# Kernel tuning notes

Hardware: AMD Instinct MI355X
Metric: run time of the kernel (lower is better)

## Reference

```python
import jax, jax.numpy as jnp
import numpy as np

D = 1280        # embed_dim
H = 20          # num heads
HD = D // H     # head_dim = 64
FFN = 5120
SEQ = 4096
NSEG = 8
EPS = 1e-5


def _ln(x, g, b):
    mu = jnp.mean(x, axis=-1, keepdims=True)
    var = jnp.var(x, axis=-1, keepdims=True)
    return (x - mu) * jax.lax.rsqrt(var + EPS) * g + b


def setup_inputs() -> dict:
    key = jax.random.key(0)
    ks = jax.random.split(key, 16)
    s = 0.02
    inp = {
        "hidden_states": jax.random.normal(ks[0], (SEQ, D), dtype=jnp.float32),
        "cu_seqlens": jnp.arange(NSEG + 1, dtype=jnp.int32) * (SEQ // NSEG),
        "Wq": jax.random.normal(ks[1], (D, D), dtype=jnp.float32) * s,
        "bq": jnp.zeros((D,), jnp.float32),
        "Wk": jax.random.normal(ks[2], (D, D), dtype=jnp.float32) * s,
        "Wv": jax.random.normal(ks[3], (D, D), dtype=jnp.float32) * s,
        "bv": jnp.zeros((D,), jnp.float32),
        "Wo": jax.random.normal(ks[4], (D, D), dtype=jnp.float32) * s,
        "bo": jnp.zeros((D,), jnp.float32),
        "ln1_g": jnp.ones((D,), jnp.float32),
        "ln1_b": jnp.zeros((D,), jnp.float32),
        "Wf1": jax.random.normal(ks[5], (D, FFN), dtype=jnp.float32) * s,
        "bf1": jnp.zeros((FFN,), jnp.float32),
        "Wf2": jax.random.normal(ks[6], (FFN, D), dtype=jnp.float32) * s,
        "bf2": jnp.zeros((D,), jnp.float32),
        "ln2_g": jnp.ones((D,), jnp.float32),
        "ln2_b": jnp.zeros((D,), jnp.float32),
    }
    return inp


def reference(hidden_states, cu_seqlens, Wq, bq, Wk, Wv, bv, Wo, bo,
              ln1_g, ln1_b, Wf1, bf1, Wf2, bf2, ln2_g, ln2_b):
    seq = hidden_states.shape[0]
    # --- self-attention block ---
    residual = hidden_states
    x = _ln(hidden_states, ln1_g, ln1_b)
    q = (x @ Wq + bq).reshape(seq, H, HD).transpose(1, 0, 2)   # [H,S,hd]
    k = (x @ Wk).reshape(seq, H, HD).transpose(1, 0, 2)
    v = (x @ Wv + bv).reshape(seq, H, HD).transpose(1, 0, 2)
    scores = jnp.einsum('hqd,hkd->hqk', q, k) / jnp.sqrt(jnp.float32(HD))
    # block-diagonal mask from cu_seqlens (segment id per token)
    pos = jnp.arange(seq, dtype=jnp.int32)
    seg = jnp.searchsorted(cu_seqlens, pos, side='right')      # [S]
    same = seg[None, :, None] == seg[None, None, :]            # [1,S,S]
    neg = jnp.finfo(scores.dtype).min
    scores = jnp.where(same, scores, scores + neg)
    attn = jax.nn.softmax(scores, axis=-1)
    attn_out = jnp.einsum('hqk,hkd->hqd', attn, v).transpose(1, 0, 2).reshape(seq, D)
    attn_out = attn_out @ Wo + bo
    h = residual + attn_out
    # --- FFN block ---
    residual = h
    y = _ln(h, ln2_g, ln2_b)
    y = jax.nn.gelu(y @ Wf1 + bf1, approximate=False)
    y = y @ Wf2 + bf2
    return residual + y
```

## Files before the change

kernel.cpp:

```cpp
#include <hip/hip_runtime.h>
#include <cstdint>
#include <cstddef>

#define SEQ_ 4096
#define DIM_ 1280
#define NHEAD_ 20
#define HDIM_ 64
#define FFN_ 5120
#define SEG_ 512
#define QKVN_ 3840

typedef __attribute__((ext_vector_type(8))) short bf16x8;
typedef __attribute__((ext_vector_type(4))) float f32x4;
typedef __attribute__((ext_vector_type(8))) unsigned short us8;
typedef __attribute__((ext_vector_type(4))) unsigned short us4;

__device__ __forceinline__ unsigned short f2b(float f) {
  unsigned int u = __builtin_bit_cast(unsigned int, f);
  u += 0x7fffu + ((u >> 16) & 1u);
  return (unsigned short)(u >> 16);
}

__device__ __forceinline__ float b2f(unsigned short u) {
  return __builtin_bit_cast(float, (unsigned int)u << 16);
}

__device__ __forceinline__ void gload_lds16(const void* g, void* l) {
  __builtin_amdgcn_global_load_lds(
      (const __attribute__((address_space(1))) unsigned int*)g,
      (__attribute__((address_space(3))) unsigned int*)l, 16, 0, 0);
}

#define WAITVM(N) asm volatile("s_waitcnt vmcnt(" #N ")" ::: "memory")

__global__ __launch_bounds__(256) void transp_all_kernel(
    const float* __restrict__ Wq, const float* __restrict__ Wk,
    const float* __restrict__ Wv, const float* __restrict__ Wo,
    const float* __restrict__ Wf1, const float* __restrict__ Wf2,
    unsigned short* __restrict__ Wqkvt, unsigned short* __restrict__ Wot,
    unsigned short* __restrict__ Wf1t, unsigned short* __restrict__ Wf2t) {
  __shared__ float tile[32][33];
  int t = blockIdx.x;
  const float* in;
  unsigned short* out;
  int R, C, bx, by;
  if (t < 6400) {
    int m = t / 1600, lt = t - m * 1600;
    in = (m == 0) ? Wq : (m == 1) ? Wk : (m == 2) ? Wv : Wo;
    out = (m < 3) ? Wqkvt + (size_t)m * DIM_ * DIM_ : Wot;
    R = DIM_; C = DIM_;
    bx = lt % 40; by = lt / 40;
  } else if (t < 12800) {
    int lt = t - 6400;
    in = Wf1; out = Wf1t; R = DIM_; C = FFN_;
    bx = lt % 160; by = lt / 160;
  } else {
    int lt = t - 12800;
    in = Wf2; out = Wf2t; R = FFN_; C = DIM_;
    bx = lt % 40; by = lt / 40;
  }
  int c0 = bx * 32, r0 = by * 32;
  int tx = threadIdx.x & 31, ty = threadIdx.x >> 5;
#pragma unroll
  for (int i = 0; i < 32; i += 8)
    tile[ty + i][tx] = in[(size_t)(r0 + ty + i) * C + c0 + tx];
  __syncthreads();
#pragma unroll
  for (int i = 0; i < 32; i += 8)
    out[(size_t)(c0 + ty + i) * R + r0 + tx] = f2b(tile[tx][ty + i]);
}

__global__ __launch_bounds__(256) void ln_kernel(
    const float* __restrict__ in, const float* __restrict__ g,
    const float* __restrict__ b, unsigned short* __restrict__ out) {
  int row = blockIdx.x, tid = threadIdx.x;
  int l = tid & 63, w = tid >> 6;
  const float* x = in + (size_t)row * DIM_;
  float v[5], s = 0.f, s2 = 0.f;
#pragma unroll
  for (int i = 0; i < 5; ++i) {
    v[i] = x[tid + i * 256];
    s += v[i];
    s2 += v[i] * v[i];
  }
#pragma unroll
  for (int off = 1; off < 64; off <<= 1) {
    s += __shfl_xor(s, off);
    s2 += __shfl_xor(s2, off);
  }
  __shared__ float red[8];
  if (l == 0) { red[w * 2] = s; red[w * 2 + 1] = s2; }
  __syncthreads();
  s = red[0] + red[2] + red[4] + red[6];
  s2 = red[1] + red[3] + red[5] + red[7];
  float mu = s * (1.f / DIM_);
  float var = s2 * (1.f / DIM_) - mu * mu;
  float rs = rsqrtf(var + 1e-5f);
#pragma unroll
  for (int i = 0; i < 5; ++i) {
    int c = tid + i * 256;
    out[(size_t)row * DIM_ + c] = f2b((v[i] - mu) * rs * g[c] + b[c]);
  }
}

enum { EPI_QKV = 0, EPI_GELU = 3, EPI_PART = 4 };

template <int EPI>
__device__ __forceinline__ void gemm_body(
    const unsigned short* __restrict__ A, int lda,
    const unsigned short* __restrict__ Bt, int ldb,
    const float* __restrict__ bias, const float* __restrict__ bias2,
    void* __restrict__ out0, void* __restrict__ out1, void* __restrict__ out2,
    int M, int N, int K, int nz) {
  __shared__ char lds[3][24576];
  const int tid = threadIdx.x;
  const int l = tid & 63, w = tid >> 6;
  const int r16 = l & 15, kg4 = l >> 4;
  const int nx = gridDim.x;
  const int orig = blockIdx.y * nx + blockIdx.x;
  const int xcd = orig & 7, idx = orig >> 3;
  const int by = xcd * (gridDim.y >> 3) + idx / nx;
  const int bx = idx % nx;
  const int m0 = by * 128, n0 = bx * 256;
  const int wm = (w >> 2) * 64, wn = (w & 3) * 64;
  const int z = blockIdx.z;
  const int ntK = K >> 5;
  const int base = ntK / nz, rem = ntK % nz;
  const int k0 = z * base + (z < rem ? z : rem);
  const int nt = base + (z < rem ? 1 : 0);
  const int kc = (tid & 3) ^ ((tid >> 3) & 3);
  const unsigned short* aA = A + (size_t)(m0 + (tid >> 2)) * lda + kc * 8 + k0 * 32;
  const unsigned short* aB = Bt + (size_t)(n0 + (tid >> 2)) * ldb + kc * 8 + k0 * 32;
  const unsigned short* aB1 = aB + (size_t)128 * ldb;
  const int cswz = (kg4 ^ ((r16 >> 1) & 3)) << 4;
  int aoff[4], boff[4];
#pragma unroll
  for (int mi = 0; mi < 4; ++mi) aoff[mi] = (wm + mi * 16 + r16) * 64 + cswz;
#pragma unroll
  for (int ni = 0; ni < 4; ++ni) boff[ni] = 8192 + (wn + ni * 16 + r16) * 64 + cswz;

  f32x4 acc[4][4] = {};

#define STAGE(b, kt_)                                          \
  do {                                                         \
    const int kb = (kt_) * 32;                                 \
    char* dA = &lds[0][0] + (b) * 24576 + w * 1024;            \
    char* dB = dA + 8192;                                      \
    gload_lds16(aA + kb, dA);                                  \
    gload_lds16(aB + kb, dB);                                  \
    gload_lds16(aB1 + kb, dB + 8192);                          \
  } while (0)

  STAGE(0, 0);
  if (nt > 1) {
    STAGE(1, 1);
    WAITVM(3);
  } else {
    WAITVM(0);
  }
  __builtin_amdgcn_s_barrier();

  int cur = 0;
#pragma unroll 1
  for (int t = 0; t < nt; ++t) {
    if (t + 2 < nt) {
      int nxt = cur + 2; if (nxt >= 3) nxt -= 3;
      STAGE(nxt, t + 2);
    }
    const char* sl = &lds[0][0] + cur * 24576;
    bf16x8 af[4], bfv[4];
#pragma unroll
    for (int mi = 0; mi < 4; ++mi) af[mi] = *(const bf16x8*)(sl + aoff[mi]);
#pragma unroll
    for (int ni = 0; ni < 4; ++ni) bfv[ni] = *(const bf16x8*)(sl + boff[ni]);
    __builtin_amdgcn_s_setprio(1);
#pragma unroll
    for (int mi = 0; mi < 4; ++mi)
#pragma unroll
      for (int ni = 0; ni < 4; ++ni)
        acc[mi][ni] = __builtin_amdgcn_mfma_f32_16x16x32_bf16(af[mi], bfv[ni], acc[mi][ni], 0, 0, 0);
    __builtin_amdgcn_s_setprio(0);
    if (t + 2 < nt) WAITVM(3);
    else if (t + 1 < nt) WAITVM(0);
    if (t + 1 < nt) __builtin_amdgcn_s_barrier();
    ++cur; if (cur == 3) cur = 0;
  }
#undef STAGE

  const int rg = kg4 * 4;
#pragma unroll
  for (int mi = 0; mi < 4; ++mi) {
#pragma unroll
    for (int ni = 0; ni < 4; ++ni) {
      int row = m0 + wm + mi * 16 + rg;
      int col = n0 + wn + ni * 16 + r16;
      f32x4 v = acc[mi][ni];
      if constexpr (EPI == EPI_QKV) {
        if (col < DIM_) {
          unsigned short* O = (unsigned short*)out0;
          float bb = bias[col];
#pragma unroll
          for (int j = 0; j < 4; ++j) O[(size_t)(row + j) * DIM_ + col] = f2b(v[j] + bb);
        } else if (col < 2 * DIM_) {
          unsigned short* O = (unsigned short*)out1;
          int cc = col - DIM_;
#pragma unroll
          for (int j = 0; j < 4; ++j) O[(size_t)(row + j) * DIM_ + cc] = f2b(v[j]);
        } else {
          unsigned short* O = (unsigned short*)out2;
          int cc = col - 2 * DIM_;
          float bb = bias2[cc];
          us4 pk;
#pragma unroll
          for (int j = 0; j < 4; ++j) pk[j] = f2b(v[j] + bb);
          *(us4*)(O + (size_t)cc * SEQ_ + row) = pk;
        }
      } else if constexpr (EPI == EPI_GELU) {
        unsigned short* O = (unsigned short*)out0;
        float bb = bias[col];
#pragma unroll
        for (int j = 0; j < 4; ++j) {
          float t = v[j] + bb;
          t = 0.5f * t * (1.f + erff(t * 0.70710678118f));
          O[(size_t)(row + j) * N + col] = f2b(t);
        }
      } else {
        float* O = (float*)out0 + (size_t)blockIdx.z * M * N;
#pragma unroll
        for (int j = 0; j < 4; ++j) O[(size_t)(row + j) * N + col] = v[j];
      }
    }
  }
}

__global__ __launch_bounds__(512, 4) void qkv_gemm(
    const unsigned short* A, const unsigned short* Bt, const float* bq,
    const float* bv, void* q, void* k, void* v) {
  gemm_body<EPI_QKV>(A, DIM_, Bt, DIM_, bq, bv, q, k, v, SEQ_, QKVN_, DIM_, 1);
}
__global__ __launch_bounds__(512, 4) void wo_gemm(
    const unsigned short* A, const unsigned short* Bt, void* part) {
  gemm_body<EPI_PART>(A, DIM_, Bt, DIM_, nullptr, nullptr, part, nullptr, nullptr,
                      SEQ_, DIM_, DIM_, 3);
}
__global__ __launch_bounds__(512, 4) void ffn1_gemm(
    const unsigned short* A, const unsigned short* Bt, const float* bf1, void* g) {
  gemm_body<EPI_GELU>(A, DIM_, Bt, DIM_, bf1, nullptr, g, nullptr, nullptr,
                      SEQ_, FFN_, DIM_, 1);
}
__global__ __launch_bounds__(512, 4) void ffn2_gemm(
    const unsigned short* A, const unsigned short* Bt, void* part) {
  gemm_body<EPI_PART>(A, FFN_, Bt, FFN_, nullptr, nullptr, part, nullptr, nullptr,
                      SEQ_, DIM_, FFN_, 3);
}

__global__ __launch_bounds__(256) void reduce3_kernel(
    const float* __restrict__ part, const float* __restrict__ bias,
    const float* __restrict__ res, float* __restrict__ out) {
  const size_t MN = (size_t)SEQ_ * DIM_;
  for (size_t i = blockIdx.x * 256 + threadIdx.x; i * 4 < MN; i += (size_t)gridDim.x * 256) {
    size_t e = i * 4;
    f32x4 a = *(const f32x4*)(part + e);
    f32x4 b = *(const f32x4*)(part + MN + e);
    f32x4 c = *(const f32x4*)(part + 2 * MN + e);
    f32x4 r = *(const f32x4*)(res + e);
    f32x4 bb = *(const f32x4*)(bias + (int)(e % DIM_));
    f32x4 o = a + b + c + r + bb;
    *(f32x4*)(out + e) = o;
  }
}

__global__ __launch_bounds__(256) void reduce3_ln_kernel(
    const float* __restrict__ part, const float* __restrict__ bias,
    const float* __restrict__ res, const float* __restrict__ g,
    const float* __restrict__ b, float* __restrict__ hout,
    unsigned short* __restrict__ yout) {
  const size_t MN = (size_t)SEQ_ * DIM_;
  int row = blockIdx.x, tid = threadIdx.x;
  int l = tid & 63, w = tid >> 6;
  float v[5], s = 0.f, s2 = 0.f;
#pragma unroll
  for (int i = 0; i < 5; ++i) {
    int c = tid + i * 256;
    size_t e = (size_t)row * DIM_ + c;
    float t = part[e] + part[MN + e] + part[2 * MN + e] + bias[c] + res[e];
    hout[e] = t;
    v[i] = t;
    s += t;
    s2 += t * t;
  }
#pragma unroll
  for (int off = 1; off < 64; off <<= 1) {
    s += __shfl_xor(s, off);
    s2 += __shfl_xor(s2, off);
  }
  __shared__ float red[8];
  if (l == 0) { red[w * 2] = s; red[w * 2 + 1] = s2; }
  __syncthreads();
  s = red[0] + red[2] + red[4] + red[6];
  s2 = red[1] + red[3] + red[5] + red[7];
  float mu = s * (1.f / DIM_);
  float var = s2 * (1.f / DIM_) - mu * mu;
  float rs = rsqrtf(var + 1e-5f);
#pragma unroll
  for (int i = 0; i < 5; ++i) {
    int c = tid + i * 256;
    yout[(size_t)row * DIM_ + c] = f2b((v[i] - mu) * rs * g[c] + b[c]);
  }
}

__global__ __launch_bounds__(256) void attn_kernel(
    const unsigned short* __restrict__ Q, const unsigned short* __restrict__ Kb,
    const unsigned short* __restrict__ Vt, unsigned short* __restrict__ O) {
  __shared__ unsigned short S[64][512];
  int tid = threadIdx.x;
  int l = tid & 63, w = tid >> 6;
  int orig = blockIdx.x;
  int b = (orig & 7) * (gridDim.x >> 3) + (orig >> 3);
  int qc = b & 7, seg = (b >> 3) & 7, hh = b >> 6;
  int r16 = l & 15, kg = l >> 4, rg = (l >> 4) * 4;
  int qrow0 = seg * SEG_ + qc * 64 + w * 16;
  bf16x8 aq[2];
#pragma unroll
  for (int ks = 0; ks < 2; ++ks)
    aq[ks] = *(const bf16x8*)(Q + (size_t)(qrow0 + r16) * DIM_ + hh * HDIM_ + ks * 32 + kg * 8);
#pragma unroll 4
  for (int kc = 0; kc < 32; ++kc) {
    f32x4 acc = {};
    __builtin_amdgcn_s_setprio(1);
#pragma unroll
    for (int ks = 0; ks < 2; ++ks) {
      bf16x8 bk = *(const bf16x8*)(Kb + (size_t)(seg * SEG_ + kc * 16 + r16) * DIM_ +
                                   hh * HDIM_ + ks * 32 + kg * 8);
      acc = __builtin_amdgcn_mfma_f32_16x16x32_bf16(aq[ks], bk, acc, 0, 0, 0);
    }
    __builtin_amdgcn_s_setprio(0);
#pragma unroll
    for (int j = 0; j < 4; ++j)
      S[w * 16 + rg + j][kc * 16 + r16] = f2b(acc[j] * 0.125f);
  }
#pragma unroll 2
  for (int r = 0; r < 16; ++r) {
    unsigned short* Sr = &S[w * 16 + r][0];
    us8 raw = *(const us8*)(Sr + l * 8);
    float ev[8];
#pragma unroll
    for (int j = 0; j < 8; ++j) ev[j] = b2f(raw[j]);
    float m = fmaxf(fmaxf(fmaxf(ev[0], ev[1]), fmaxf(ev[2], ev[3])),
                    fmaxf(fmaxf(ev[4], ev[5]), fmaxf(ev[6], ev[7])));
#pragma unroll
    for (int off = 1; off < 64; off <<= 1) m = fmaxf(m, __shfl_xor(m, off));
    float sum = 0.f;
#pragma unroll
    for (int j = 0; j < 8; ++j) { ev[j] = __expf(ev[j] - m); sum += ev[j]; }
#pragma unroll
    for (int off = 1; off < 64; off <<= 1) sum += __shfl_xor(sum, off);
    float inv = 1.f / sum;
    us8 pk;
#pragma unroll
    for (int j = 0; j < 8; ++j) pk[j] = f2b(ev[j] * inv);
    *(us8*)(Sr + ((l ^ (r & 7)) * 8)) = pk;
  }
  f32x4 oacc[4] = {};
  const unsigned short* Pr = &S[w * 16 + r16][0];
  int rowx = r16 & 7;
#pragma unroll 2
  for (int ks = 0; ks < 16; ++ks) {
    int chunk = (ks * 4 + kg) ^ rowx;
    bf16x8 pa = *(const bf16x8*)(Pr + chunk * 8);
    __builtin_amdgcn_s_setprio(1);
#pragma unroll
    for (int df = 0; df < 4; ++df) {
      bf16x8 bv = *(const bf16x8*)(Vt + (size_t)(hh * HDIM_ + df * 16 + r16) * SEQ_ +
                                   seg * SEG_ + ks * 32 + kg * 8);
      oacc[df] = __builtin_amdgcn_mfma_f32_16x16x32_bf16(pa, bv, oacc[df], 0, 0, 0);
    }
    __builtin_amdgcn_s_setprio(0);
  }
#pragma unroll
  for (int df = 0; df < 4; ++df)
#pragma unroll
    for (int j = 0; j < 4; ++j)
      O[(size_t)(qrow0 + rg + j) * DIM_ + hh * HDIM_ + df * 16 + r16] = f2b(oacc[df][j]);
}

extern "C" void kernel_launch(void* const* d_in, const int* in_sizes, int n_in,
                              void* d_out, int out_size, void* d_ws, size_t ws_size,
                              hipStream_t stream) {
  (void)in_sizes; (void)n_in; (void)out_size; (void)ws_size;
  const float* hidden = (const float*)d_in[0];
  const float* Wq = (const float*)d_in[2];
  const float* bq = (const float*)d_in[3];
  const float* Wk = (const float*)d_in[4];
  const float* Wv = (const float*)d_in[5];
  const float* bv = (const float*)d_in[6];
  const float* Wo = (const float*)d_in[7];
  const float* bo = (const float*)d_in[8];
  const float* g1 = (const float*)d_in[9];
  const float* b1 = (const float*)d_in[10];
  const float* Wf1 = (const float*)d_in[11];
  const float* bf1 = (const float*)d_in[12];
  const float* Wf2 = (const float*)d_in[13];
  const float* bf2 = (const float*)d_in[14];
  const float* g2 = (const float*)d_in[15];
  const float* b2 = (const float*)d_in[16];

  char* p = (char*)d_ws;
  auto alloc = [&](size_t bytes) {
    char* r = p;
    p += (bytes + 255) & ~(size_t)255;
    return r;
  };
  unsigned short* xln   = (unsigned short*)alloc((size_t)SEQ_ * DIM_ * 2);
  unsigned short* Wqkvt = (unsigned short*)alloc((size_t)DIM_ * QKVN_ * 2);
  unsigned short* Wot   = (unsigned short*)alloc((size_t)DIM_ * DIM_ * 2);
  unsigned short* Wf1t  = (unsigned short*)alloc((size_t)DIM_ * FFN_ * 2);
  unsigned short* Wf2t  = (unsigned short*)alloc((size_t)DIM_ * FFN_ * 2);
  unsigned short* Qb    = (unsigned short*)alloc((size_t)SEQ_ * DIM_ * 2);
  unsigned short* Kbf   = (unsigned short*)alloc((size_t)SEQ_ * DIM_ * 2);
  unsigned short* Vtb   = (unsigned short*)alloc((size_t)SEQ_ * DIM_ * 2);
  unsigned short* attnb = (unsigned short*)alloc((size_t)SEQ_ * DIM_ * 2);
  float*          hbuf  = (float*)alloc((size_t)SEQ_ * DIM_ * 4);
  unsigned short* ybuf  = (unsigned short*)alloc((size_t)SEQ_ * DIM_ * 2);
  unsigned short* gbuf  = (unsigned short*)alloc((size_t)SEQ_ * FFN_ * 2);
  float*          part3 = (float*)alloc((size_t)3 * SEQ_ * DIM_ * 4);

  transp_all_kernel<<<19200, 256, 0, stream>>>(
      Wq, Wk, Wv, Wo, Wf1, Wf2, Wqkvt, Wot, Wf1t, Wf2t);
  ln_kernel<<<SEQ_, 256, 0, stream>>>(hidden, g1, b1, xln);
  qkv_gemm<<<dim3(QKVN_ / 256, SEQ_ / 128), 512, 0, stream>>>(
      xln, Wqkvt, bq, bv, Qb, Kbf, Vtb);
  attn_kernel<<<NHEAD_ * 8 * 8, 256, 0, stream>>>(Qb, Kbf, Vtb, attnb);
  wo_gemm<<<dim3(DIM_ / 256, SEQ_ / 128, 3), 512, 0, stream>>>(attnb, Wot, part3);
  reduce3_ln_kernel<<<SEQ_, 256, 0, stream>>>(part3, bo, hidden, g2, b2, hbuf, ybuf);
  ffn1_gemm<<<dim3(FFN_ / 256, SEQ_ / 128), 512, 0, stream>>>(ybuf, Wf1t, bf1, gbuf);
  ffn2_gemm<<<dim3(DIM_ / 256, SEQ_ / 128, 3), 512, 0, stream>>>(gbuf, Wf2t, part3);
  reduce3_kernel<<<2048, 256, 0, stream>>>(part3, bf2, hbuf, (float*)d_out);
}
```

Baseline: 383.8 us.

## Store split-K partials in bf16 and fuse LN1 into transpose kernel

The split-K partial sums from the Wo and FFN2 GEMMs are now written as bf16 instead of fp32, and the two reduce kernels widen them back to float. This halves the write and read traffic for the partial buffer. Separately, the first layernorm is folded into the weight-transpose launch as extra blocks, removing one kernel launch. Rounding partial sums to bf16 before the reduction adds numerical error in the residual path.

```diff
diff --git a/kernel.cpp b/kernel.cpp
--- a/kernel.cpp
+++ b/kernel.cpp
@@ -33,14 +33,47 @@
 
 #define WAITVM(N) asm volatile("s_waitcnt vmcnt(" #N ")" ::: "memory")
 
-__global__ __launch_bounds__(256) void transp_all_kernel(
+__global__ __launch_bounds__(256) void transp_ln_kernel(
     const float* __restrict__ Wq, const float* __restrict__ Wk,
     const float* __restrict__ Wv, const float* __restrict__ Wo,
     const float* __restrict__ Wf1, const float* __restrict__ Wf2,
     unsigned short* __restrict__ Wqkvt, unsigned short* __restrict__ Wot,
-    unsigned short* __restrict__ Wf1t, unsigned short* __restrict__ Wf2t) {
+    unsigned short* __restrict__ Wf1t, unsigned short* __restrict__ Wf2t,
+    const float* __restrict__ hidden, const float* __restrict__ g1,
+    const float* __restrict__ b1, unsigned short* __restrict__ xln) {
+  int t = blockIdx.x;
+  if (t >= 19200) {
+    int row = t - 19200, tid = threadIdx.x;
+    int l = tid & 63, w = tid >> 6;
+    const float* x = hidden + (size_t)row * DIM_;
+    float v[5], s = 0.f, s2 = 0.f;
+#pragma unroll
+    for (int i = 0; i < 5; ++i) {
+      v[i] = x[tid + i * 256];
+      s += v[i];
+      s2 += v[i] * v[i];
+    }
+#pragma unroll
+    for (int off = 1; off < 64; off <<= 1) {
+      s += __shfl_xor(s, off);
+      s2 += __shfl_xor(s2, off);
+    }
+    __shared__ float red[8];
+    if (l == 0) { red[w * 2] = s; red[w * 2 + 1] = s2; }
+    __syncthreads();
+    s = red[0] + red[2] + red[4] + red[6];
+    s2 = red[1] + red[3] + red[5] + red[7];
+    float mu = s * (1.f / DIM_);
+    float var = s2 * (1.f / DIM_) - mu * mu;
+    float rs = rsqrtf(var + 1e-5f);
+#pragma unroll
+    for (int i = 0; i < 5; ++i) {
+      int c = tid + i * 256;
+      xln[(size_t)row * DIM_ + c] = f2b((v[i] - mu) * rs * g1[c] + b1[c]);
+    }
+    return;
+  }
   __shared__ float tile[32][33];
-  int t = blockIdx.x;
   const float* in;
   unsigned short* out;
   int R, C, bx, by;
@@ -68,39 +101,6 @@
 #pragma unroll
   for (int i = 0; i < 32; i += 8)
     out[(size_t)(c0 + ty + i) * R + r0 + tx] = f2b(tile[tx][ty + i]);
-}
-
-__global__ __launch_bounds__(256) void ln_kernel(
-    const float* __restrict__ in, const float* __restrict__ g,
-    const float* __restrict__ b, unsigned short* __restrict__ out) {
-  int row = blockIdx.x, tid = threadIdx.x;
-  int l = tid & 63, w = tid >> 6;
-  const float* x = in + (size_t)row * DIM_;
-  float v[5], s = 0.f, s2 = 0.f;
-#pragma unroll
-  for (int i = 0; i < 5; ++i) {
-    v[i] = x[tid + i * 256];
-    s += v[i];
-    s2 += v[i] * v[i];
-  }
-#pragma unroll
-  for (int off = 1; off < 64; off <<= 1) {
-    s += __shfl_xor(s, off);
-    s2 += __shfl_xor(s2, off);
-  }
-  __shared__ float red[8];
-  if (l == 0) { red[w * 2] = s; red[w * 2 + 1] = s2; }
-  __syncthreads();
-  s = red[0] + red[2] + red[4] + red[6];
-  s2 = red[1] + red[3] + red[5] + red[7];
-  float mu = s * (1.f / DIM_);
-  float var = s2 * (1.f / DIM_) - mu * mu;
-  float rs = rsqrtf(var + 1e-5f);
-#pragma unroll
-  for (int i = 0; i < 5; ++i) {
-    int c = tid + i * 256;
-    out[(size_t)row * DIM_ + c] = f2b((v[i] - mu) * rs * g[c] + b[c]);
-  }
 }
 
 enum { EPI_QKV = 0, EPI_GELU = 3, EPI_PART = 4 };
@@ -225,9 +225,9 @@
           O[(size_t)(row + j) * N + col] = f2b(t);
         }
       } else {
-        float* O = (float*)out0 + (size_t)blockIdx.z * M * N;
-#pragma unroll
-        for (int j = 0; j < 4; ++j) O[(size_t)(row + j) * N + col] = v[j];
+        unsigned short* O = (unsigned short*)out0 + (size_t)blockIdx.z * M * N;
+#pragma unroll
+        for (int j = 0; j < 4; ++j) O[(size_t)(row + j) * N + col] = f2b(v[j]);
       }
     }
   }
@@ -255,23 +255,25 @@
 }
 
 __global__ __launch_bounds__(256) void reduce3_kernel(
-    const float* __restrict__ part, const float* __restrict__ bias,
+    const unsigned short* __restrict__ part, const float* __restrict__ bias,
     const float* __restrict__ res, float* __restrict__ out) {
   const size_t MN = (size_t)SEQ_ * DIM_;
   for (size_t i = blockIdx.x * 256 + threadIdx.x; i * 4 < MN; i += (size_t)gridDim.x * 256) {
     size_t e = i * 4;
-    f32x4 a = *(const f32x4*)(part + e);
-    f32x4 b = *(const f32x4*)(part + MN + e);
-    f32x4 c = *(const f32x4*)(part + 2 * MN + e);
+    us4 a = *(const us4*)(part + e);
+    us4 b = *(const us4*)(part + MN + e);
+    us4 c = *(const us4*)(part + 2 * MN + e);
     f32x4 r = *(const f32x4*)(res + e);
     f32x4 bb = *(const f32x4*)(bias + (int)(e % DIM_));
-    f32x4 o = a + b + c + r + bb;
+    f32x4 o;
+#pragma unroll
+    for (int j = 0; j < 4; ++j) o[j] = b2f(a[j]) + b2f(b[j]) + b2f(c[j]) + r[j] + bb[j];
     *(f32x4*)(out + e) = o;
   }
 }
 
 __global__ __launch_bounds__(256) void reduce3_ln_kernel(
-    const float* __restrict__ part, const float* __restrict__ bias,
+    const unsigned short* __restrict__ part, const float* __restrict__ bias,
     const float* __restrict__ res, const float* __restrict__ g,
     const float* __restrict__ b, float* __restrict__ hout,
     unsigned short* __restrict__ yout) {
@@ -283,7 +285,7 @@
   for (int i = 0; i < 5; ++i) {
     int c = tid + i * 256;
     size_t e = (size_t)row * DIM_ + c;
-    float t = part[e] + part[MN + e] + part[2 * MN + e] + bias[c] + res[e];
+    float t = b2f(part[e]) + b2f(part[MN + e]) + b2f(part[2 * MN + e]) + bias[c] + res[e];
     hout[e] = t;
     v[i] = t;
     s += t;
@@ -423,11 +425,10 @@
   float*          hbuf  = (float*)alloc((size_t)SEQ_ * DIM_ * 4);
   unsigned short* ybuf  = (unsigned short*)alloc((size_t)SEQ_ * DIM_ * 2);
   unsigned short* gbuf  = (unsigned short*)alloc((size_t)SEQ_ * FFN_ * 2);
-  float*          part3 = (float*)alloc((size_t)3 * SEQ_ * DIM_ * 4);
-
-  transp_all_kernel<<<19200, 256, 0, stream>>>(
-      Wq, Wk, Wv, Wo, Wf1, Wf2, Wqkvt, Wot, Wf1t, Wf2t);
-  ln_kernel<<<SEQ_, 256, 0, stream>>>(hidden, g1, b1, xln);
+  unsigned short* part3 = (unsigned short*)alloc((size_t)3 * SEQ_ * DIM_ * 2);
+
+  transp_ln_kernel<<<19200 + SEQ_, 256, 0, stream>>>(
+      Wq, Wk, Wv, Wo, Wf1, Wf2, Wqkvt, Wot, Wf1t, Wf2t, hidden, g1, b1, xln);
   qkv_gemm<<<dim3(QKVN_ / 256, SEQ_ / 128), 512, 0, stream>>>(
       xln, Wqkvt, bq, bv, Qb, Kbf, Vtb);
   attn_kernel<<<NHEAD_ * 8 * 8, 256, 0, stream>>>(Qb, Kbf, Vtb, attnb);
```

Measured after the change: 367.7 us. -4.2%, faster.
